# Kernel optimization log

Hardware: AMD Instinct MI355X
Metric: run time of the kernel (lower is better)

The kernel has to match this reference:

```python
import jax, jax.numpy as jnp
import numpy as np

H, D, K, FF = 8, 512, 64, 64  # n_head, feature_dim, key_feature_dim, dim_feedforward
L, B = 512, 32
LN_EPS = 1e-5


def _l2norm(x, eps=1e-12):
    # torch F.normalize: x / max(||x||, eps)
    n = jnp.sqrt(jnp.sum(x * x, axis=-1, keepdims=True))
    return x / jnp.maximum(n, eps)


def _layernorm(x, g, b, eps=LN_EPS):
    m = jnp.mean(x, axis=-1, keepdims=True)
    v = jnp.mean((x - m) ** 2, axis=-1, keepdims=True)
    return (x - m) * jax.lax.rsqrt(v + eps) * g + b


def setup_inputs() -> dict:
    key0 = jax.random.key(0)
    ks = jax.random.split(key0, 13)
    n = jax.random.normal
    s_kq = float(np.sqrt(2.0 / K))
    s_v = float(np.sqrt(2.0 / D))
    return {
        "query": n(ks[0], (L, B, D), jnp.float32),
        "key": n(ks[1], (L, B, D), jnp.float32),
        "value": n(ks[2], (L, B, D), jnp.float32),
        "WK": n(ks[3], (H, K, D), jnp.float32) * s_kq,
        "WQ": n(ks[4], (H, K, D), jnp.float32) * s_kq,
        "WV": n(ks[5], (H, D, D), jnp.float32) * s_v,
        "Wt": n(ks[6], (H, D, D), jnp.float32) * 0.04,  # trans_conv (default kaiming-ish scale)
        "W1": n(ks[7], (H, FF, D), jnp.float32) * 0.04,
        "b1": jnp.zeros((H, FF), jnp.float32),
        "W2": n(ks[8], (H, D, FF), jnp.float32) * 0.1,
        "b2": jnp.zeros((H, D), jnp.float32),
        "ln_g": jnp.ones((H, D), jnp.float32),
        "ln_b": jnp.zeros((H, D), jnp.float32),
    }


def reference(query, key, value, WK, WQ, WV, Wt, W1, b1, W2, b2, ln_g, ln_b):
    # query/key/value: [L, B, D]; per-head weights stacked on leading H axis.
    Lq, Bb, Dd = query.shape
    Hh = WK.shape[0]

    # per-head cosine-normalized Q/K projections: [H, B, L, K]
    wq = _l2norm(jnp.einsum('lbd,hkd->hblk', query, WQ))
    wk = _l2norm(jnp.einsum('lbd,hkd->hblk', key, WK))

    # attention scores [H, B, Lq, Lk], temp = 1
    dot = jnp.einsum('hbqc,hbkc->hbqk', wq, wk)
    aff = jax.nn.softmax(dot, axis=-1)
    # custom renorm: divide by column sums over the QUERY axis
    aff = aff / (1e-9 + jnp.sum(aff, axis=2, keepdims=True))

    wv = jnp.einsum('lbd,hed->hble', value, WV)        # [H, B, Lk, D]
    out = jnp.einsum('hbqk,hbke->hbqe', aff, wv)       # [H, B, Lq, D]
    out = jnp.transpose(out, (0, 2, 1, 3))             # [H, L, B, D]

    # residual-style trans_conv(query - out) -> relu
    o = jax.nn.relu(jnp.einsum('hlbd,hed->hlbe', query[None] - out, Wt))

    # TransNonlinear FFN (dropout = identity at eval)
    hff = jax.nn.relu(jnp.einsum('hlbd,hfd->hlbf', o, W1) + b1[:, None, None, :])
    s2 = jnp.einsum('hlbf,hdf->hlbd', hff, W2) + b2[:, None, None, :]
    x = _layernorm(o + s2, ln_g[:, None, None, :], ln_b[:, None, None, :])

    # concat heads on last dim, head 0 first: [L, B, H*D]
    return jnp.transpose(x, (1, 2, 0, 3)).reshape(Lq, Bb, Hh * Dd)
```

## Files before the change

kernel.cpp:

```cpp
#include <hip/hip_runtime.h>
#include <stdint.h>

#define HH 8
#define DDIM 512
#define KHEAD 64
#define FFD 64
#define LLEN 512
#define BBATCH 32
#define NTOK 16384

typedef unsigned short u16;
typedef __attribute__((ext_vector_type(8))) __bf16 bf16x8;
typedef __attribute__((ext_vector_type(4))) float f32x4;

__device__ __forceinline__ float bf2f(u16 u) {
    union { uint32_t i; float f; } v; v.i = ((uint32_t)u) << 16; return v.f;
}
__device__ __forceinline__ u16 f2bf(float f) {
    union { uint32_t i; float f; } v; v.f = f;
    return (u16)((v.i + 0x7FFFu + ((v.i >> 16) & 1u)) >> 16);
}

__device__ __forceinline__ void gload16(const void* g, void* l) {
    __builtin_amdgcn_global_load_lds(
        (const __attribute__((address_space(1))) void*)g,
        (__attribute__((address_space(3))) void*)l, 16, 0, 0);
}

__global__ __launch_bounds__(256) void f2bf4(const float* __restrict__ in,
                                             u16* __restrict__ out, int n4) {
    int i = blockIdx.x * 256 + threadIdx.x;
    if (i >= n4) return;
    float4 v = ((const float4*)in)[i];
    ushort4 o; o.x = f2bf(v.x); o.y = f2bf(v.y); o.z = f2bf(v.z); o.w = f2bf(v.w);
    ((ushort4*)out)[i] = o;
}

enum { M_PLAIN = 0, M_WQK = 1, M_SUBAUX = 2, M_RELU = 3, M_ADDAUX = 4, M_SCALECOL = 5 };

template<int BM, int BN, int MODE, int ZMAP, int SWAPXY>
__global__ __launch_bounds__(256) void mgemm(
    const u16* __restrict__ A, const u16* __restrict__ B, u16* __restrict__ C,
    int Kd, int lda, int ldb, int ldc,
    long Ash, long Asb, long Bsh, long Bsb, long Csh, long Csb, int nB2,
    const float* __restrict__ bias, int biasN,
    const void* __restrict__ auxp, long auxsh, long auxsb, int auxld)
{
    constexpr int WC = (BN == 128) ? 2 : 1;
    constexpr int WR = 4 / WC;
    constexpr int WTM = BM / WR;
    constexpr int WTN = BN / WC;
    constexpr int MF = WTM / 16;
    constexpr int NF = WTN / 16;
    constexpr int NCA = (BM * 64) / 4096;
    constexpr int NCB = (BN * 64) / 4096;
    __shared__ u16 As[2][BM * 32];
    __shared__ u16 Bs[2][BN * 32];

    const int z = blockIdx.z;
    int h2, b2;
    if (ZMAP == 0)      { h2 = z / nB2;      b2 = z % nB2; }
    else if (ZMAP == 1) { h2 = z & 7;        b2 = z >> 3; }
    else                { h2 = (z >> 3) & 7; b2 = ((z >> 6) << 3) | (z & 7); }
    const u16* Ab = A + h2 * Ash + b2 * Asb;
    const u16* Bb = B + h2 * Bsh + b2 * Bsb;
    const int bx = SWAPXY ? blockIdx.y : blockIdx.x;
    const int by = SWAPXY ? blockIdx.x : blockIdx.y;
    const int m0 = bx * BM, n0 = by * BN;
    const int t = threadIdx.x;
    const int lane = t & 63;
    const int w = t >> 6;
    const int wr = w / WC, wc = w % WC;
    const int tb = t * 16;
    const int wb = (t & 192) * 16;

    f32x4 acc[MF][NF];
    #pragma unroll
    for (int m = 0; m < MF; ++m)
        #pragma unroll
        for (int n = 0; n < NF; ++n)
            #pragma unroll
            for (int i = 0; i < 4; ++i) acc[m][n][i] = 0.f;

    const int ko = (lane >> 4) * 16;

    auto stage = [&](int buf, int k0) {
        #pragma unroll
        for (int c = 0; c < NCA; ++c) {
            const int byte = c * 4096 + tb;
            const int row = byte >> 6;
            gload16((const char*)(Ab + (long)(m0 + row) * lda + k0) + (byte & 63),
                    (char*)As[buf] + c * 4096 + wb);
        }
        #pragma unroll
        for (int c = 0; c < NCB; ++c) {
            const int byte = c * 4096 + tb;
            const int row = byte >> 6;
            gload16((const char*)(Bb + (long)(n0 + row) * ldb + k0) + (byte & 63),
                    (char*)Bs[buf] + c * 4096 + wb);
        }
    };

    stage(0, 0);
    __syncthreads();
    int cur = 0;
    const int nsteps = Kd >> 5;
    for (int s = 0; s < nsteps; ++s) {
        if (s + 1 < nsteps) stage(cur ^ 1, (s + 1) << 5);
        bf16x8 af[MF], bfr[NF];
        #pragma unroll
        for (int m = 0; m < MF; ++m)
            af[m] = *(const bf16x8*)((const char*)As[cur] + (wr * WTM + m * 16 + (lane & 15)) * 64 + ko);
        #pragma unroll
        for (int n = 0; n < NF; ++n)
            bfr[n] = *(const bf16x8*)((const char*)Bs[cur] + (wc * WTN + n * 16 + (lane & 15)) * 64 + ko);
        #pragma unroll
        for (int m = 0; m < MF; ++m)
            #pragma unroll
            for (int n = 0; n < NF; ++n)
                acc[m][n] = __builtin_amdgcn_mfma_f32_16x16x32_bf16(af[m], bfr[n], acc[m][n], 0, 0, 0);
        __syncthreads();
        cur ^= 1;
    }

    const int lr = (lane >> 4) * 4;
    const int lc = lane & 15;

    if constexpr (MODE == M_WQK) {
        const int h = (n0 + wc * WTN) >> 6;
        #pragma unroll
        for (int m = 0; m < MF; ++m) {
            #pragma unroll
            for (int i = 0; i < 4; ++i) {
                float s = 0.f;
                #pragma unroll
                for (int n = 0; n < NF; ++n) { const float v = acc[m][n][i]; s += v * v; }
                s += __shfl_xor(s, 1); s += __shfl_xor(s, 2);
                s += __shfl_xor(s, 4); s += __shfl_xor(s, 8);
                const float inv = 1.0f / fmaxf(sqrtf(s), 1e-12f);
                const int r = m0 + wr * WTM + m * 16 + lr + i;
                const int l = r >> 5, bq = r & 31;
                const int sw = (l & 7) << 3;
                u16* rowp = C + (((long)(h * BBATCH + bq) * LLEN + l) * KHEAD);
                #pragma unroll
                for (int n = 0; n < NF; ++n)
                    rowp[(lc + n * 16) ^ sw] = f2bf(acc[m][n][i] * inv);
            }
        }
    } else {
        const long cof = h2 * Csh + b2 * Csb;
        #pragma unroll
        for (int m = 0; m < MF; ++m) {
            #pragma unroll
            for (int i = 0; i < 4; ++i) {
                const int r = m0 + wr * WTM + m * 16 + lr + i;
                #pragma unroll
                for (int n = 0; n < NF; ++n) {
                    const int c = n0 + wc * WTN + n * 16 + lc;
                    float v = acc[m][n][i];
                    if (MODE == M_SUBAUX) {
                        const u16* q = (const u16*)auxp;
                        v = bf2f(q[auxsh * h2 + auxsb * b2 + (long)r * auxld + c]) - v;
                    } else if (MODE == M_RELU) {
                        if (bias) v += bias[h2 * biasN + c];
                        v = fmaxf(v, 0.0f);
                    } else if (MODE == M_ADDAUX) {
                        v += bias[h2 * biasN + c];
                        const u16* ax = (const u16*)auxp;
                        v += bf2f(ax[auxsh * h2 + auxsb * b2 + (long)r * auxld + c]);
                    } else if (MODE == M_SCALECOL) {
                        const float* cs = (const float*)auxp + auxsh * h2 + auxsb * b2;
                        v *= 1.0f / (1e-9f + cs[c]);
                    }
                    C[cof + (long)r * ldc + c] = f2bf(v);
                }
            }
        }
    }
}

__global__ __launch_bounds__(256) void attn_mfma(
    const u16* __restrict__ wq, const u16* __restrict__ wk,
    u16* __restrict__ P, float* __restrict__ colsum)
{
    __shared__ u16 qs[64 * 64];
    __shared__ u16 ks[512 * 64];
    __shared__ float smax[4][64];
    __shared__ float ssum[4][64];

    const int qt = blockIdx.x, b = blockIdx.y, h = blockIdx.z;
    const long hb = h * BBATCH + b;
    const int t = threadIdx.x;
    const int lane = t & 63, w = t >> 6;
    const int wb = (t & 192) * 16;

    const char* qg = (const char*)(wq + (hb * LLEN + qt * 64) * KHEAD);
    const char* kg = (const char*)(wk + hb * LLEN * KHEAD);
    #pragma unroll
    for (int c = 0; c < 2; ++c)
        gload16(qg + c * 4096 + t * 16, (char*)qs + c * 4096 + wb);
    #pragma unroll
    for (int c = 0; c < 16; ++c)
        gload16(kg + c * 4096 + t * 16, (char*)ks + c * 4096 + wb);
    __syncthreads();

    const int l15 = lane & 15;
    const int g = lane >> 4;
    const int swz = (lane & 7) << 4;

    f32x4 acc[4][8];
    #pragma unroll
    for (int m = 0; m < 4; ++m)
        #pragma unroll
        for (int n = 0; n < 8; ++n)
            #pragma unroll
            for (int i = 0; i < 4; ++i) acc[m][n][i] = 0.f;

    #pragma unroll
    for (int kk = 0; kk < 2; ++kk) {
        bf16x8 af[4];
        #pragma unroll
        for (int m = 0; m < 4; ++m) {
            const int row = m * 16 + l15;
            af[m] = *(const bf16x8*)((const char*)qs + row * 128 + ((g * 16 + kk * 64) ^ swz));
        }
        #pragma unroll
        for (int n = 0; n < 8; ++n) {
            const int row = (w * 8 + n) * 16 + l15;
            const bf16x8 bfr = *(const bf16x8*)((const char*)ks + row * 128 + ((g * 16 + kk * 64) ^ swz));
            #pragma unroll
            for (int m = 0; m < 4; ++m)
                acc[m][n] = __builtin_amdgcn_mfma_f32_16x16x32_bf16(af[m], bfr, acc[m][n], 0, 0, 0);
        }
    }

    float rmax[4][4];
    #pragma unroll
    for (int m = 0; m < 4; ++m)
        #pragma unroll
        for (int i = 0; i < 4; ++i) {
            float mx = acc[m][0][i];
            #pragma unroll
            for (int n = 1; n < 8; ++n) mx = fmaxf(mx, acc[m][n][i]);
            mx = fmaxf(mx, __shfl_xor(mx, 1));
            mx = fmaxf(mx, __shfl_xor(mx, 2));
            mx = fmaxf(mx, __shfl_xor(mx, 4));
            mx = fmaxf(mx, __shfl_xor(mx, 8));
            if (l15 == 0) smax[w][m * 16 + g * 4 + i] = mx;
        }
    __syncthreads();
    #pragma unroll
    for (int m = 0; m < 4; ++m)
        #pragma unroll
        for (int i = 0; i < 4; ++i) {
            const int r = m * 16 + g * 4 + i;
            rmax[m][i] = fmaxf(fmaxf(smax[0][r], smax[1][r]),
                               fmaxf(smax[2][r], smax[3][r]));
        }
    float rinv[4][4];
    #pragma unroll
    for (int m = 0; m < 4; ++m)
        #pragma unroll
        for (int i = 0; i < 4; ++i) {
            float s = 0.f;
            #pragma unroll
            for (int n = 0; n < 8; ++n) {
                acc[m][n][i] = __expf(acc[m][n][i] - rmax[m][i]);
                s += acc[m][n][i];
            }
            s += __shfl_xor(s, 1); s += __shfl_xor(s, 2);
            s += __shfl_xor(s, 4); s += __shfl_xor(s, 8);
            if (l15 == 0) ssum[w][m * 16 + g * 4 + i] = s;
        }
    __syncthreads();
    #pragma unroll
    for (int m = 0; m < 4; ++m)
        #pragma unroll
        for (int i = 0; i < 4; ++i) {
            const int r = m * 16 + g * 4 + i;
            rinv[m][i] = 1.0f / (ssum[0][r] + ssum[1][r] + ssum[2][r] + ssum[3][r]);
        }

    u16* Pb = P + (hb * LLEN + qt * 64) * LLEN + w * 128;
    float cs[8];
    #pragma unroll
    for (int n = 0; n < 8; ++n) cs[n] = 0.f;
    #pragma unroll
    for (int m = 0; m < 4; ++m)
        #pragma unroll
        for (int i = 0; i < 4; ++i) {
            const int r = m * 16 + g * 4 + i;
            u16* pr = Pb + (long)r * LLEN + l15;
            const float iv = rinv[m][i];
            #pragma unroll
            for (int n = 0; n < 8; ++n) {
                const float p = acc[m][n][i] * iv;
                pr[n * 16] = f2bf(p);
                cs[n] += p;
            }
        }
    #pragma unroll
    for (int n = 0; n < 8; ++n) {
        cs[n] += __shfl_xor(cs[n], 16);
        cs[n] += __shfl_xor(cs[n], 32);
    }
    if (lane < 16) {
        float* cb = colsum + hb * 512 + w * 128 + lane;
        #pragma unroll
        for (int n = 0; n < 8; ++n) atomicAdd(&cb[n * 16], cs[n]);
    }
}

__global__ __launch_bounds__(256) void ffn2_ln(
    const u16* __restrict__ hff, const u16* __restrict__ W2bf,
    const float* __restrict__ b2, const u16* __restrict__ o,
    const float* __restrict__ lng, const float* __restrict__ lnb,
    float* __restrict__ out)
{
    __shared__ u16 W2s[512 * 64];
    __shared__ u16 hs[32 * 64];
    __shared__ float redS[4][32];
    __shared__ float redQ[4][32];

    const int h = blockIdx.z;
    const int m0 = blockIdx.x * 32;
    const int t = threadIdx.x;
    const int lane = t & 63, w = t >> 6;
    const int l15 = lane & 15, g = lane >> 4;
    const int wb = (t & 192) * 16;

    const char* w2g = (const char*)W2bf + (long)h * 65536;
    #pragma unroll
    for (int c = 0; c < 16; ++c)
        gload16(w2g + c * 4096 + t * 16, (char*)W2s + c * 4096 + wb);
    gload16((const char*)hff + ((long)h * NTOK + m0) * 128 + t * 16, (char*)hs + wb);
    __syncthreads();

    f32x4 acc[2][8];
    #pragma unroll
    for (int m = 0; m < 2; ++m)
        #pragma unroll
        for (int n = 0; n < 8; ++n)
            #pragma unroll
            for (int i = 0; i < 4; ++i) acc[m][n][i] = 0.f;

    #pragma unroll
    for (int kk = 0; kk < 2; ++kk) {
        bf16x8 af[2];
        #pragma unroll
        for (int m = 0; m < 2; ++m)
            af[m] = *(const bf16x8*)((const char*)hs + (m * 16 + l15) * 128 + kk * 64 + g * 16);
        #pragma unroll
        for (int n = 0; n < 8; ++n) {
            const int e = w * 128 + n * 16 + l15;
            const bf16x8 bfr = *(const bf16x8*)((const char*)W2s + e * 128 + kk * 64 + g * 16);
            #pragma unroll
            for (int m = 0; m < 2; ++m)
                acc[m][n] = __builtin_amdgcn_mfma_f32_16x16x32_bf16(af[m], bfr, acc[m][n], 0, 0, 0);
        }
    }

    float b2v[8], gv[8], bv[8];
    #pragma unroll
    for (int n = 0; n < 8; ++n) {
        const int c = w * 128 + n * 16 + l15;
        b2v[n] = b2[h * DDIM + c];
        gv[n] = lng[h * DDIM + c];
        bv[n] = lnb[h * DDIM + c];
    }
    const u16* ob = o + ((long)h * NTOK + m0) * DDIM;
    #pragma unroll
    for (int m = 0; m < 2; ++m)
        #pragma unroll
        for (int i = 0; i < 4; ++i) {
            const int row = m * 16 + g * 4 + i;
            float s = 0.f, q = 0.f;
            #pragma unroll
            for (int n = 0; n < 8; ++n) {
                const int c = w * 128 + n * 16 + l15;
                const float v = acc[m][n][i] + b2v[n] + bf2f(ob[(long)row * DDIM + c]);
                acc[m][n][i] = v;
                s += v; q += v * v;
            }
            s += __shfl_xor(s, 1); q += __shfl_xor(q, 1);
            s += __shfl_xor(s, 2); q += __shfl_xor(q, 2);
            s += __shfl_xor(s, 4); q += __shfl_xor(q, 4);
            s += __shfl_xor(s, 8); q += __shfl_xor(q, 8);
            if (l15 == 0) { redS[w][row] = s; redQ[w][row] = q; }
        }
    __syncthreads();

    #pragma unroll
    for (int m = 0; m < 2; ++m)
        #pragma unroll
        for (int i = 0; i < 4; ++i) {
            const int row = m * 16 + g * 4 + i;
            const float s = redS[0][row] + redS[1][row] + redS[2][row] + redS[3][row];
            const float q = redQ[0][row] + redQ[1][row] + redQ[2][row] + redQ[3][row];
            const float mu = s * (1.0f / 512.0f);
            const float var = q * (1.0f / 512.0f) - mu * mu;
            const float rs = rsqrtf(var + 1e-5f);
            const int tok = m0 + row;
            const int b = tok >> 9, l = tok & 511;
            float* op = out + ((long)(l * BBATCH + b)) * (HH * DDIM) + h * DDIM;
            #pragma unroll
            for (int n = 0; n < 8; ++n) {
                const int c = w * 128 + n * 16 + l15;
                op[c] = (acc[m][n][i] - mu) * rs * gv[n] + bv[n];
            }
        }
}

extern "C" void kernel_launch(void* const* d_in, const int* in_sizes, int n_in,
                              void* d_out, int out_size, void* d_ws, size_t ws_size,
                              hipStream_t stream) {
    const float* query = (const float*)d_in[0];
    const float* key   = (const float*)d_in[1];
    const float* value = (const float*)d_in[2];
    const float* WK = (const float*)d_in[3];
    const float* WQ = (const float*)d_in[4];
    const float* WV = (const float*)d_in[5];
    const float* Wt = (const float*)d_in[6];
    const float* W1 = (const float*)d_in[7];
    const float* b1 = (const float*)d_in[8];
    const float* W2 = (const float*)d_in[9];
    const float* b2 = (const float*)d_in[10];
    const float* lng = (const float*)d_in[11];
    const float* lnb = (const float*)d_in[12];

    char* ws = (char*)d_ws;
    u16* kbf  = (u16*)(ws);
    u16* WQbf = (u16*)(ws + 16777216);
    u16* WKbf = (u16*)(ws + 17301504);
    u16* P    = (u16*)(ws);
    u16* vbf  = (u16*)(ws + 134217728);
    u16* WVbf = (u16*)(ws + 150994944);
    u16* o    = (u16*)(ws + 134217728);
    float* colsum = (float*)(ws + 268435456);
    u16* qbf  = (u16*)(ws + 268959744);
    u16* hff  = qbf;
    u16* wq   = (u16*)(ws + 285736960);
    u16* wk   = (u16*)(ws + 302514176);
    u16* Wtbf = (u16*)(ws + 285736960);
    u16* W1bf = (u16*)(ws + 289931264);
    u16* W2bf = (u16*)(ws + 290455552);
    u16* qmo = (u16*)d_out;
    u16* wvT = (u16*)((char*)d_out + 134217728);

    if (ws_size < 319291392u) return;

    hipMemsetAsync(colsum, 0, 524288, stream);
    const dim3 blk(256);

    f2bf4<<<dim3(8192), blk, 0, stream>>>(query, qbf, 2097152);
    f2bf4<<<dim3(8192), blk, 0, stream>>>(key,   kbf, 2097152);
    f2bf4<<<dim3(8192), blk, 0, stream>>>(value, vbf, 2097152);
    f2bf4<<<dim3(256),  blk, 0, stream>>>(WQ, WQbf, 65536);
    f2bf4<<<dim3(256),  blk, 0, stream>>>(WK, WKbf, 65536);
    f2bf4<<<dim3(2048), blk, 0, stream>>>(WV, WVbf, 524288);

    mgemm<128, 128, M_WQK, 0, 1><<<dim3(4, 128, 1), blk, 0, stream>>>(
        qbf, WQbf, wq, 512, 512, 512, 0,
        0, 0, 0, 0, 0, 0, 1, nullptr, 0, nullptr, 0, 0, 0);
    mgemm<128, 128, M_WQK, 0, 1><<<dim3(4, 128, 1), blk, 0, stream>>>(
        kbf, WKbf, wk, 512, 512, 512, 0,
        0, 0, 0, 0, 0, 0, 1, nullptr, 0, nullptr, 0, 0, 0);

    attn_mfma<<<dim3(8, 32, 8), blk, 0, stream>>>(wq, wk, P, colsum);

    f2bf4<<<dim3(2048), blk, 0, stream>>>(Wt, Wtbf, 524288);
    f2bf4<<<dim3(256),  blk, 0, stream>>>(W1, W1bf, 65536);
    f2bf4<<<dim3(256),  blk, 0, stream>>>(W2, W2bf, 65536);

    mgemm<128, 128, M_SCALECOL, 2, 0><<<dim3(4, 4, 256), blk, 0, stream>>>(
        WVbf, vbf, wvT, 512, 512, BBATCH * DDIM, 512,
        (long)DDIM * DDIM, 0, 0, DDIM,
        (long)BBATCH * DDIM * LLEN, (long)DDIM * LLEN, 32,
        nullptr, 0, colsum, (long)BBATCH * 512, 512, 0);

    mgemm<128, 128, M_SUBAUX, 1, 0><<<dim3(4, 4, 256), blk, 0, stream>>>(
        P, wvT, qmo, 512, 512, 512, 512,
        (long)BBATCH * LLEN * LLEN, (long)LLEN * LLEN,
        (long)BBATCH * DDIM * LLEN, (long)DDIM * LLEN,
        (long)BBATCH * LLEN * DDIM, (long)LLEN * DDIM, 32,
        nullptr, 0, qbf, 0, DDIM, BBATCH * DDIM);

    mgemm<128, 128, M_RELU, 0, 1><<<dim3(4, 128, 8), blk, 0, stream>>>(
        qmo, Wtbf, o, 512, 512, 512, 512,
        (long)NTOK * DDIM, 0, (long)DDIM * DDIM, 0,
        (long)NTOK * DDIM, 0, 1, nullptr, 512, nullptr, 0, 0, 0);

    mgemm<128, 64, M_RELU, 0, 0><<<dim3(128, 1, 8), blk, 0, stream>>>(
        o, W1bf, hff, 512, 512, 512, 64,
        (long)NTOK * DDIM, 0, (long)FFD * DDIM, 0,
        (long)NTOK * FFD, 0, 1, b1, 64, nullptr, 0, 0, 0);

    ffn2_ln<<<dim3(512, 1, 8), blk, 0, stream>>>(hff, W2bf, b2, o, lng, lnb,
                                                 (float*)d_out);
}
```

Baseline: 771.8 us.

## Batch conversion launches, remap attention blocks for XCD locality, swizzle FFN2 LDS

Result: no change. 766.2 us (-0.7%).

```diff
diff --git a/kernel.cpp b/kernel.cpp
--- a/kernel.cpp
+++ b/kernel.cpp
@@ -27,13 +27,22 @@
         (__attribute__((address_space(3))) void*)l, 16, 0, 0);
 }
 
-__global__ __launch_bounds__(256) void f2bf4(const float* __restrict__ in,
-                                             u16* __restrict__ out, int n4) {
-    int i = blockIdx.x * 256 + threadIdx.x;
-    if (i >= n4) return;
-    float4 v = ((const float4*)in)[i];
-    ushort4 o; o.x = f2bf(v.x); o.y = f2bf(v.y); o.z = f2bf(v.z); o.w = f2bf(v.w);
-    ((ushort4*)out)[i] = o;
+struct ConvJob { const float* s; u16* d; int n4; };
+struct ConvJobs { ConvJob j[6]; int nj; };
+
+__global__ __launch_bounds__(256) void conv_multi(ConvJobs jobs) {
+    for (int k = 0; k < jobs.nj; ++k) {
+        const float* s = jobs.j[k].s;
+        u16* d = jobs.j[k].d;
+        const int n4 = jobs.j[k].n4;
+        for (long i = (long)blockIdx.x * 256 + threadIdx.x; i < n4;
+             i += (long)gridDim.x * 256) {
+            float4 v = ((const float4*)s)[i];
+            ushort4 o;
+            o.x = f2bf(v.x); o.y = f2bf(v.y); o.z = f2bf(v.z); o.w = f2bf(v.w);
+            ((ushort4*)d)[i] = o;
+        }
+    }
 }
 
 enum { M_PLAIN = 0, M_WQK = 1, M_SUBAUX = 2, M_RELU = 3, M_ADDAUX = 4, M_SCALECOL = 5 };
@@ -179,6 +188,14 @@
     }
 }
 
+__device__ __forceinline__ void xcd_decode(int wgid, int& qt, int& b, int& h) {
+    const int r = wgid & 7;
+    const int inner = wgid >> 3;
+    qt = inner & 7;
+    h = (inner >> 3) & 7;
+    b = ((inner >> 6) << 3) | r;
+}
+
 __global__ __launch_bounds__(256) void attn_mfma(
     const u16* __restrict__ wq, const u16* __restrict__ wk,
     u16* __restrict__ P, float* __restrict__ colsum)
@@ -188,7 +205,8 @@
     __shared__ float smax[4][64];
     __shared__ float ssum[4][64];
 
-    const int qt = blockIdx.x, b = blockIdx.y, h = blockIdx.z;
+    int qt, b, h;
+    xcd_decode(blockIdx.x, qt, b, h);
     const long hb = h * BBATCH + b;
     const int t = threadIdx.x;
     const int lane = t & 63, w = t >> 6;
@@ -331,9 +349,21 @@
 
     const char* w2g = (const char*)W2bf + (long)h * 65536;
     #pragma unroll
-    for (int c = 0; c < 16; ++c)
-        gload16(w2g + c * 4096 + t * 16, (char*)W2s + c * 4096 + wb);
-    gload16((const char*)hff + ((long)h * NTOK + m0) * 128 + t * 16, (char*)hs + wb);
+    for (int c = 0; c < 16; ++c) {
+        const int idx = c * 4096 + t * 16;
+        const int row = idx >> 7;
+        const int g0 = (idx >> 4) & 7;
+        gload16(w2g + row * 128 + ((g0 ^ (row & 7)) << 4),
+                (char*)W2s + c * 4096 + wb);
+    }
+    {
+        const int idx = t * 16;
+        const int row = idx >> 7;
+        const int g0 = (idx >> 4) & 7;
+        gload16((const char*)(hff + ((long)h * NTOK + m0) * FFD) +
+                    row * 128 + ((g0 ^ (row & 7)) << 4),
+                (char*)hs + wb);
+    }
     __syncthreads();
 
     f32x4 acc[2][8];
@@ -348,12 +378,16 @@
     for (int kk = 0; kk < 2; ++kk) {
         bf16x8 af[2];
         #pragma unroll
-        for (int m = 0; m < 2; ++m)
-            af[m] = *(const bf16x8*)((const char*)hs + (m * 16 + l15) * 128 + kk * 64 + g * 16);
+        for (int m = 0; m < 2; ++m) {
+            const int row = m * 16 + l15;
+            af[m] = *(const bf16x8*)((const char*)hs + row * 128 +
+                                     (((kk * 4 + g) ^ (row & 7)) << 4));
+        }
         #pragma unroll
         for (int n = 0; n < 8; ++n) {
             const int e = w * 128 + n * 16 + l15;
-            const bf16x8 bfr = *(const bf16x8*)((const char*)W2s + e * 128 + kk * 64 + g * 16);
+            const bf16x8 bfr = *(const bf16x8*)((const char*)W2s + e * 128 +
+                                                (((kk * 4 + g) ^ (e & 7)) << 4));
             #pragma unroll
             for (int m = 0; m < 2; ++m)
                 acc[m][n] = __builtin_amdgcn_mfma_f32_16x16x32_bf16(af[m], bfr, acc[m][n], 0, 0, 0);
@@ -452,12 +486,17 @@
     hipMemsetAsync(colsum, 0, 524288, stream);
     const dim3 blk(256);
 
-    f2bf4<<<dim3(8192), blk, 0, stream>>>(query, qbf, 2097152);
-    f2bf4<<<dim3(8192), blk, 0, stream>>>(key,   kbf, 2097152);
-    f2bf4<<<dim3(8192), blk, 0, stream>>>(value, vbf, 2097152);
-    f2bf4<<<dim3(256),  blk, 0, stream>>>(WQ, WQbf, 65536);
-    f2bf4<<<dim3(256),  blk, 0, stream>>>(WK, WKbf, 65536);
-    f2bf4<<<dim3(2048), blk, 0, stream>>>(WV, WVbf, 524288);
+    {
+        ConvJobs J;
+        J.j[0] = { query, qbf, 2097152 };
+        J.j[1] = { key,   kbf, 2097152 };
+        J.j[2] = { value, vbf, 2097152 };
+        J.j[3] = { WQ, WQbf, 65536 };
+        J.j[4] = { WK, WKbf, 65536 };
+        J.j[5] = { WV, WVbf, 524288 };
+        J.nj = 6;
+        conv_multi<<<dim3(2048), blk, 0, stream>>>(J);
+    }
 
     mgemm<128, 128, M_WQK, 0, 1><<<dim3(4, 128, 1), blk, 0, stream>>>(
         qbf, WQbf, wq, 512, 512, 512, 0,
@@ -466,11 +505,16 @@
         kbf, WKbf, wk, 512, 512, 512, 0,
         0, 0, 0, 0, 0, 0, 1, nullptr, 0, nullptr, 0, 0, 0);
 
-    attn_mfma<<<dim3(8, 32, 8), blk, 0, stream>>>(wq, wk, P, colsum);
-
-    f2bf4<<<dim3(2048), blk, 0, stream>>>(Wt, Wtbf, 524288);
-    f2bf4<<<dim3(256),  blk, 0, stream>>>(W1, W1bf, 65536);
-    f2bf4<<<dim3(256),  blk, 0, stream>>>(W2, W2bf, 65536);
+    attn_mfma<<<dim3(2048), blk, 0, stream>>>(wq, wk, P, colsum);
+
+    {
+        ConvJobs J;
+        J.j[0] = { Wt, Wtbf, 524288 };
+        J.j[1] = { W1, W1bf, 65536 };
+        J.j[2] = { W2, W2bf, 65536 };
+        J.nj = 3;
+        conv_multi<<<dim3(1024), blk, 0, stream>>>(J);
+    }
 
     mgemm<128, 128, M_SCALECOL, 2, 0><<<dim3(4, 4, 256), blk, 0, stream>>>(
         WVbf, vbf, wvT, 512, 512, BBATCH * DDIM, 512,
```
